# Performance work log

Measured on AMD Instinct MI355X. Metric: run time of the kernel, lower is better.

## Reference

```python
import jax, jax.numpy as jnp
import numpy as np

EPS_IN = 1e-5  # torch InstanceNorm1d default eps


def instance_norm(x):
    # x: [B, C, L]; normalize over L per (B, C); no affine (torch default)
    m = jnp.mean(x, axis=-1, keepdims=True)
    v = jnp.var(x, axis=-1, keepdims=True)
    return (x - m) / jnp.sqrt(v + EPS_IN)


def conv1x1(x, w, b):
    # x: [B, Cin, L], w: [Cout, Cin], b: [Cout]
    return jnp.einsum('bcl,oc->bol', x, w) + b[None, :, None]


def _window_indices(L_dec, L_enc, window, stride):
    # static (numpy) window layout matching the torch while-loop
    starts = list(range(0, L_dec, stride))
    dec_ends = [min(s + window, L_dec) for s in starts]
    enc_se = [(int(s * L_enc / L_dec), min(int(e * L_enc / L_dec), L_enc))
              for s, e in zip(starts, dec_ends)]
    max_enc = max(ee - es for es, ee in enc_se)
    ar_d = np.arange(window)
    ar_e = np.arange(max_enc)
    dec_idx = np.stack([np.clip(s + ar_d, 0, L_dec - 1) for s in starts])          # [NW, Wd]
    dec_valid = np.stack([(s + ar_d) < e for s, e in zip(starts, dec_ends)])       # [NW, Wd]
    enc_idx = np.stack([np.clip(es + ar_e, 0, L_enc - 1) for es, ee in enc_se])    # [NW, We]
    enc_valid = np.stack([(es + ar_e) < ee for es, ee in enc_se])                  # [NW, We]
    return (jnp.asarray(dec_idx), jnp.asarray(dec_valid),
            jnp.asarray(enc_idx), jnp.asarray(enc_valid))


def setup_inputs() -> dict:
    key = jax.random.key(0)
    ks = jax.random.split(key, 16)
    B, Cd, Ce, Ld, Le = 4, 512, 256, 4096, 8192
    H = 4 * Cd  # mlp hidden
    s = 0.02
    return {
        'x_decoder': jax.random.normal(ks[0], (B, Cd, Ld), jnp.float32),
        'x_encoder': jax.random.normal(ks[1], (B, Ce, Le), jnp.float32),
        'wq': jax.random.normal(ks[2], (Cd, Cd), jnp.float32) * s,
        'bq': jnp.zeros((Cd,), jnp.float32),
        'wk': jax.random.normal(ks[3], (Cd, Ce), jnp.float32) * s,
        'bk': jnp.zeros((Cd,), jnp.float32),
        'wv': jax.random.normal(ks[4], (Cd, Ce), jnp.float32) * s,
        'bv': jnp.zeros((Cd,), jnp.float32),
        'wo': jax.random.normal(ks[5], (Cd, Cd), jnp.float32) * s,
        'bo': jnp.zeros((Cd,), jnp.float32),
        'w1': jax.random.normal(ks[6], (H, Cd), jnp.float32) * s,
        'b1': jnp.zeros((H,), jnp.float32),
        'w2': jax.random.normal(ks[7], (Cd, H), jnp.float32) * s,
        'b2': jnp.zeros((Cd,), jnp.float32),
    }


NUM_HEADS = 8
WINDOW = 256
STRIDE = 192  # int(256 * (1 - 0.25))


def reference(x_decoder, x_encoder, wq, bq, wk, bk, wv, bv, wo, bo, w1, b1, w2, b2):
    B, Cd, Ld = x_decoder.shape
    Le = x_encoder.shape[-1]
    nh, hd = NUM_HEADS, Cd // NUM_HEADS
    residual = x_decoder

    q = instance_norm(conv1x1(x_decoder, wq, bq))
    k = instance_norm(conv1x1(x_encoder, wk, bk))
    v = instance_norm(conv1x1(x_encoder, wv, bv))

    # [B, C, L] -> [B, nh, L, hd]
    q = q.reshape(B, nh, hd, Ld).transpose(0, 1, 3, 2)
    k = k.reshape(B, nh, hd, Le).transpose(0, 1, 3, 2)
    v = v.reshape(B, nh, hd, Le).transpose(0, 1, 3, 2)

    dec_idx, dec_valid, enc_idx, enc_valid = _window_indices(Ld, Le, WINDOW, STRIDE)
    # gather all windows at once
    qw = q[:, :, dec_idx, :]  # [B, nh, NW, Wd, hd]
    kw = k[:, :, enc_idx, :]  # [B, nh, NW, We, hd]
    vw = v[:, :, enc_idx, :]

    scale = hd ** -0.5
    scores = jnp.einsum('bhnqd,bhnkd->bhnqk', qw, kw) * scale
    scores = jnp.where(enc_valid[None, None, :, None, :], scores, jnp.float32(-1e30))
    attn = jax.nn.softmax(scores, axis=-1)
    win = jnp.einsum('bhnqk,bhnkd->bhnqd', attn, vw)
    win = win * dec_valid[None, None, :, :, None].astype(win.dtype)

    # scatter-add overlapping windows then average by overlap count
    flat_idx = dec_idx.reshape(-1)  # [NW*Wd]
    out = jnp.zeros((B, nh, Ld, hd), win.dtype).at[:, :, flat_idx, :].add(
        win.reshape(B, nh, -1, hd))
    counts = jnp.zeros((Ld,), win.dtype).at[flat_idx].add(
        dec_valid.reshape(-1).astype(win.dtype))
    out = out / jnp.clip(counts, 1e-8)[None, None, :, None]

    attn_out = out.transpose(0, 1, 3, 2).reshape(B, Cd, Ld)
    x = instance_norm(conv1x1(attn_out, wo, bo)) + residual

    # AttentionMLP1D (dropout inactive in eval)
    h = jax.nn.gelu(conv1x1(x, w1, b1), approximate=False)
    y = instance_norm(conv1x1(h, w2, b2))
    return y + x
```

## Files before the change

### kernel.cpp

```cpp
#include <hip/hip_runtime.h>
#include <hip/hip_bf16.h>
#include <math.h>
#include <stdint.h>

#define LDD 4096
#define LEE 8192
#define CDIM 512
#define CENC 256
#define HDIM 2048
#define NB 4
#define NHEAD 8
#define HD 64
#define NWIN 22
#define WINQ 256
#define WSTRIDE 192

typedef __attribute__((ext_vector_type(8))) short bf16x8;
typedef __attribute__((ext_vector_type(8))) unsigned short u16x8;
typedef __attribute__((ext_vector_type(4))) float f32x4;
typedef __attribute__((ext_vector_type(16))) float f32x16;
typedef __attribute__((ext_vector_type(2))) unsigned int u32x2;
typedef __attribute__((ext_vector_type(4))) unsigned int u32x4;
typedef unsigned short ushort_t;

__device__ __forceinline__ uint32_t pack2(float lo, float hi) {
    return ((__float_as_uint(hi) + 0x8000u) & 0xffff0000u) |
           ((__float_as_uint(lo) + 0x8000u) >> 16);
}
__device__ __forceinline__ ushort_t bfc(float x) {
    return (ushort_t)((__float_as_uint(x) + 0x8000u) >> 16);
}
__device__ __forceinline__ float bf2f(ushort_t u) {
    return __uint_as_float(((uint32_t)u) << 16);
}
__device__ __forceinline__ void gload16(const void* g, void* l) {
    __builtin_amdgcn_global_load_lds(
        (const __attribute__((address_space(1))) void*)g,
        (__attribute__((address_space(3))) void*)l, 16, 0, 0);
}
__device__ __forceinline__ float gelu_fast(float x) {
    float z = fabsf(x) * 0.70710678f;
    float t = 1.0f / fmaf(0.3275911f, z, 1.0f);
    float p = t * fmaf(t, fmaf(t, fmaf(t, fmaf(t, 1.061405429f, -1.453152027f),
                                        1.421413741f), -0.284496736f), 0.254829592f);
    float e = __expf(-z * z);
    float erfz = fmaf(-p, e, 1.0f);
    float sgn = copysignf(erfz, x);
    return 0.5f * x * (1.0f + sgn);
}

struct Cvt6Args {
    const float* src[6];
    ushort_t* dst[6];
    int n[6];
};
__global__ __launch_bounds__(256)
void cvt6(Cvt6Args a)
{
    int seg = blockIdx.y;
    int i = (blockIdx.x * 256 + threadIdx.x) * 4;
    if (i < a.n[seg]) {
        float4 v = *reinterpret_cast<const float4*>(&a.src[seg][i]);
        u32x2 p; p[0] = pack2(v.x, v.y); p[1] = pack2(v.z, v.w);
        *reinterpret_cast<u32x2*>(&a.dst[seg][i]) = p;
    }
}

__global__ __launch_bounds__(256)
void tcvt(const float* __restrict__ in, ushort_t* __restrict__ outb, int C, int L)
{
    __shared__ float T[64][65];
    int l0 = blockIdx.x * 64, c0 = blockIdx.y * 64, b = blockIdx.z;
    int tid = threadIdx.x;
    int ll = tid & 63, cq = tid >> 6;
    #pragma unroll
    for (int i = 0; i < 16; ++i) {
        int c = cq + i * 4;
        T[c][ll] = in[((size_t)b * C + c0 + c) * L + l0 + ll];
    }
    __syncthreads();
    int cc = tid & 63, lq = tid >> 6;
    #pragma unroll
    for (int i = 0; i < 16; ++i) {
        int l = lq + i * 4;
        outb[((size_t)b * L + l0 + l) * C + c0 + cc] = bfc(T[cc][l]);
    }
}

template<int EPI, int STATS>
__global__ __launch_bounds__(256)
void mgemm2(const ushort_t* __restrict__ A, const ushort_t* __restrict__ Wt,
            const float* __restrict__ bias, ushort_t* __restrict__ Out,
            float* __restrict__ part, int M, int N, int K)
{
    __shared__ __align__(16) ushort_t As[2][8192];
    __shared__ __align__(16) ushort_t Bs[2][8192];

    int Nt = gridDim.x;
    int flat = blockIdx.y * Nt + blockIdx.x;
    int nwg = Nt * gridDim.y;
    int swz = (flat & 7) * (nwg >> 3) + (flat >> 3);
    int nb = swz % Nt, mb = swz / Nt;
    int b = blockIdx.z;
    int m0 = mb * 128, n0 = nb * 128;

    int tid = threadIdx.x;
    int lane = tid & 63;
    int w = tid >> 6;
    int q16 = lane & 15, g = lane >> 4;
    int wr = w >> 1, wc = w & 1;

    const ushort_t* Ag[4]; const ushort_t* Wg[4];
    #pragma unroll
    for (int i = 0; i < 4; ++i) {
        int gran = w * 256 + i * 64 + lane;
        int row = gran >> 3;
        int c8 = (gran & 7) ^ (row & 7);
        Ag[i] = A + ((size_t)b * M + m0 + row) * K + c8 * 8;
        Wg[i] = Wt + ((size_t)(n0 + row)) * K + c8 * 8;
    }

    f32x4 acc[4][4];
    #pragma unroll
    for (int mt = 0; mt < 4; ++mt)
        #pragma unroll
        for (int nt = 0; nt < 4; ++nt) {
            acc[mt][nt][0] = 0.f; acc[mt][nt][1] = 0.f;
            acc[mt][nt][2] = 0.f; acc[mt][nt][3] = 0.f;
        }

    #pragma unroll
    for (int i = 0; i < 4; ++i) {
        gload16(Ag[i], &As[0][w * 2048 + i * 512]);
        gload16(Wg[i], &Bs[0][w * 2048 + i * 512]);
    }

    int NTILES = K >> 6;
    for (int kt = 0; kt < NTILES; ++kt) {
        int cur = kt & 1;
        __syncthreads();
        if (kt + 1 < NTILES) {
            int k0 = (kt + 1) << 6;
            #pragma unroll
            for (int i = 0; i < 4; ++i) {
                gload16(Ag[i] + k0, &As[cur ^ 1][w * 2048 + i * 512]);
                gload16(Wg[i] + k0, &Bs[cur ^ 1][w * 2048 + i * 512]);
            }
        }
        const char* Ab = (const char*)&As[cur][0];
        const char* Bb = (const char*)&Bs[cur][0];
        bf16x8 ka[4][2], kb[4][2];
        #pragma unroll
        for (int mt = 0; mt < 4; ++mt) {
            int r = wr * 64 + mt * 16 + q16;
            int rb = r * 128;
            int sw8 = (r & 7) << 4;
            ka[mt][0] = *reinterpret_cast<const bf16x8*>(Ab + rb + ((g * 16) ^ sw8));
            ka[mt][1] = *reinterpret_cast<const bf16x8*>(Ab + rb + ((64 + g * 16) ^ sw8));
        }
        #pragma unroll
        for (int nt = 0; nt < 4; ++nt) {
            int r = wc * 64 + nt * 16 + q16;
            int rb = r * 128;
            int sw8 = (r & 7) << 4;
            kb[nt][0] = *reinterpret_cast<const bf16x8*>(Bb + rb + ((g * 16) ^ sw8));
            kb[nt][1] = *reinterpret_cast<const bf16x8*>(Bb + rb + ((64 + g * 16) ^ sw8));
        }
        #pragma unroll
        for (int mt = 0; mt < 4; ++mt)
            #pragma unroll
            for (int nt = 0; nt < 4; ++nt) {
                acc[mt][nt] = __builtin_amdgcn_mfma_f32_16x16x32_bf16(kb[nt][0], ka[mt][0], acc[mt][nt], 0, 0, 0);
                acc[mt][nt] = __builtin_amdgcn_mfma_f32_16x16x32_bf16(kb[nt][1], ka[mt][1], acc[mt][nt], 0, 0, 0);
            }
    }

    float4 bv4[4];
    #pragma unroll
    for (int nt = 0; nt < 4; ++nt)
        bv4[nt] = *reinterpret_cast<const float4*>(&bias[n0 + wc * 64 + nt * 16 + g * 4]);

    float s_[4][4], q_[4][4];
    if (STATS) {
        #pragma unroll
        for (int nt = 0; nt < 4; ++nt)
            #pragma unroll
            for (int r = 0; r < 4; ++r) { s_[nt][r] = 0.f; q_[nt][r] = 0.f; }
    }

    #pragma unroll
    for (int mt = 0; mt < 4; ++mt) {
        int m = m0 + wr * 64 + mt * 16 + q16;
        size_t rowoff = ((size_t)b * M + m) * N;
        #pragma unroll
        for (int nt = 0; nt < 4; ++nt) {
            float vv[4];
            #pragma unroll
            for (int r = 0; r < 4; ++r) {
                float val = acc[mt][nt][r] + ((const float*)&bv4[nt])[r];
                if (EPI == 1) val = gelu_fast(val);
                if (STATS) { s_[nt][r] += val; q_[nt][r] = fmaf(val, val, q_[nt][r]); }
                vv[r] = val;
            }
            u32x2 pk; pk[0] = pack2(vv[0], vv[1]); pk[1] = pack2(vv[2], vv[3]);
            *reinterpret_cast<u32x2*>(&Out[rowoff + n0 + wc * 64 + nt * 16 + g * 4]) = pk;
        }
    }

    if (STATS) {
        __syncthreads();
        float* SS = (float*)&As[0][0];
        float* SQ = (float*)&Bs[0][0];
        #pragma unroll
        for (int nt = 0; nt < 4; ++nt)
            #pragma unroll
            for (int r = 0; r < 4; ++r) {
                int nl = wc * 64 + nt * 16 + g * 4 + r;
                SS[nl * 33 + wr * 16 + q16] = s_[nt][r];
                SQ[nl * 33 + wr * 16 + q16] = q_[nt][r];
            }
        __syncthreads();
        if (tid < 128) {
            float ts = 0.f, tq = 0.f;
            #pragma unroll 8
            for (int j = 0; j < 32; ++j) { ts += SS[tid * 33 + j]; tq += SQ[tid * 33 + j]; }
            size_t po = (((size_t)b * (M >> 7) + mb) * N + n0 + tid) * 2;
            part[po] = ts; part[po + 1] = tq;
        }
    }
}

__global__ __launch_bounds__(256)
void stats_finish(const float* __restrict__ pk, const float* __restrict__ pv,
                  float* __restrict__ km, float* __restrict__ kr,
                  float* __restrict__ vm, float* __restrict__ vr)
{
    int id = blockIdx.x * 256 + threadIdx.x;
    int b = id >> 9, c = id & 511;
    float sk = 0.f, qk = 0.f, sv = 0.f, qv = 0.f;
    for (int sp = 0; sp < 64; ++sp) {
        size_t po = (((size_t)(b * 64 + sp)) * CDIM + c) * 2;
        sk += pk[po]; qk += pk[po + 1];
        sv += pv[po]; qv += pv[po + 1];
    }
    float mk = sk / (float)LEE, mv = sv / (float)LEE;
    km[id] = mk;
    kr[id] = rsqrtf(qk / (float)LEE - mk * mk + 1e-5f);
    vm[id] = mv;
    vr[id] = rsqrtf(qv / (float)LEE - mv * mv + 1e-5f);
}

template<int RES>
__global__ __launch_bounds__(256)
void cn_apply_v(const ushort_t* __restrict__ in, const float* __restrict__ part,
                const ushort_t* __restrict__ res, ushort_t* __restrict__ out,
                const float* __restrict__ chscale,
                int L, int SPLITM, float oscale)
{
    __shared__ float SM[CDIM], SR[CDIM];
    int b = blockIdx.z;
    int tid = threadIdx.x;
    for (int c = tid; c < CDIM; c += 256) {
        float fs = 0.f, fq = 0.f;
        for (int sp = 0; sp < SPLITM; ++sp) {
            size_t po = (((size_t)b * SPLITM + sp) * CDIM + c) * 2;
            fs += part[po]; fq += part[po + 1];
        }
        float mean = fs / (float)L;
        float var = fq / (float)L - mean * mean;
        float sc = oscale;
        if (chscale) sc *= chscale[b * CDIM + c];
        SM[c] = mean; SR[c] = rsqrtf(var + 1e-5f) * sc;
    }
    __syncthreads();
    int c0 = (tid & 63) * 8;
    int l0 = blockIdx.x * 16 + (tid >> 6) * 4;
    float mm[8], rr[8];
    #pragma unroll
    for (int j = 0; j < 8; ++j) { mm[j] = SM[c0 + j]; rr[j] = SR[c0 + j]; }
    #pragma unroll
    for (int i = 0; i < 4; ++i) {
        int l = l0 + i;
        size_t off = ((size_t)b * L + l) * CDIM + c0;
        u16x8 v = *reinterpret_cast<const u16x8*>(in + off);
        u16x8 rv;
        if (RES) rv = *reinterpret_cast<const u16x8*>(res + off);
        u16x8 o;
        #pragma unroll
        for (int j = 0; j < 8; ++j) {
            float y = (bf2f((ushort_t)v[j]) - mm[j]) * rr[j];
            if (RES) y += bf2f((ushort_t)rv[j]);
            o[j] = bfc(y);
        }
        *reinterpret_cast<u16x8*>(out + off) = o;
    }
}

__global__ __launch_bounds__(256)
void cn_apply_t(const ushort_t* __restrict__ in, const float* __restrict__ part,
                const ushort_t* __restrict__ res, float* __restrict__ outf,
                int L, int SPLITM)
{
    __shared__ float SM[64], SR[64];
    __shared__ float T[64][65];
    int b = blockIdx.z;
    int c0 = blockIdx.x * 64;
    int l0 = blockIdx.y * 64;
    int tid = threadIdx.x;
    if (tid < 64) {
        int c = c0 + tid;
        float fs = 0.f, fq = 0.f;
        for (int sp = 0; sp < SPLITM; ++sp) {
            size_t po = (((size_t)b * SPLITM + sp) * CDIM + c) * 2;
            fs += part[po]; fq += part[po + 1];
        }
        float mean = fs / (float)L;
        float var = fq / (float)L - mean * mean;
        SM[tid] = mean; SR[tid] = rsqrtf(var + 1e-5f);
    }
    __syncthreads();
    int cc = tid & 63;
    int lq = tid >> 6;
    float mean = SM[cc], rstd = SR[cc];
    #pragma unroll
    for (int i = 0; i < 16; ++i) {
        int l = l0 + lq + i * 4;
        size_t idx = ((size_t)b * L + l) * CDIM + c0 + cc;
        T[lq + i * 4][cc] = (bf2f(in[idx]) - mean) * rstd + bf2f(res[idx]);
    }
    __syncthreads();
    int ll = tid & 63;
    int cr = tid >> 6;
    #pragma unroll
    for (int i = 0; i < 16; ++i) {
        int c = cr + i * 4;
        outf[((size_t)b * CDIM + c0 + c) * L + l0 + ll] = T[ll][c];
    }
}

__global__ __launch_bounds__(512, 2)
void attn_win_mfma32(const ushort_t* __restrict__ qT, const ushort_t* __restrict__ kT,
                     const ushort_t* __restrict__ vT,
                     const float* __restrict__ vmean, const float* __restrict__ vrstd,
                     ushort_t* __restrict__ win)
{
    __shared__ __align__(16) char KB[2][16384];
    __shared__ __align__(16) ushort_t VBv[2][64][132];
    __shared__ float VMS[64], VRS[64];

    int p = blockIdx.x;
    int xcd = p & 7;
    int sub = p >> 3;
    int g9 = xcd * 11 + (sub % 11);
    int hh = sub / 11;
    int n = g9 % 22, b = g9 / 22;

    int s = n * WSTRIDE;
    int es = 2 * s;
    bool tail = (n == NWIN - 1);
    int nch = tail ? 1 : 4;

    int tid = threadIdx.x;
    int lane = tid & 63;
    int w = tid >> 6;
    int l31 = lane & 31;
    int hf = lane >> 5;
    bool active = (!tail) || (w < 2);

    if (tid < 64) {
        int c = b * CDIM + hh * HD + tid;
        VMS[tid] = vmean[c];
        VRS[tid] = vrstd[c];
    }

    const ushort_t* kbase = kT + ((size_t)b * LEE + es) * CDIM + hh * HD;
    const ushort_t* vbase = vT + ((size_t)b * LEE + es) * CDIM + hh * HD;

    int vc8 = tid & 7;
    int vkp2 = tid >> 3;

    {
        #pragma unroll
        for (int i = 0; i < 2; ++i) {
            int gr = tid + i * 512;
            int kpos = gr >> 3;
            int c8 = (gr & 7) ^ (kpos & 7);
            gload16(kbase + (size_t)kpos * CDIM + c8 * 8, &KB[0][gr * 16]);
        }
        const ushort_t* src = vbase + (size_t)(2 * vkp2) * CDIM + vc8 * 8;
        u16x8 wa = *reinterpret_cast<const u16x8*>(src);
        u16x8 wb = *reinterpret_cast<const u16x8*>(src + CDIM);
        #pragma unroll
        for (int j = 0; j < 8; ++j) {
            int d = vc8 * 8 + j;
            uint32_t dw = (uint32_t)wa[j] | ((uint32_t)wb[j] << 16);
            *reinterpret_cast<uint32_t*>(&VBv[0][d][2 * vkp2]) = dw;
        }
    }

    bf16x8 bq[4];
    if (active) {
        int qrow_g = s + w * 32 + l31;
        const ushort_t* qp = qT + ((size_t)b * LDD + qrow_g) * CDIM + hh * HD;
        #pragma unroll
        for (int kd = 0; kd < 4; ++kd)
            bq[kd] = *reinterpret_cast<const bf16x8*>(qp + kd * 16 + hf * 8);
    }

    f32x16 acc0, acc1;
    #pragma unroll
    for (int e = 0; e < 16; ++e) { acc0[e] = 0.f; acc1[e] = 0.f; }
    float m = -3e38f, ssum = 0.f;
    int swk = (lane & 7) << 4;

    for (int ch = 0; ch < nch; ++ch) {
        int buf = ch & 1;
        __syncthreads();

        u16x8 wa, wb;
        bool pf = (ch + 1 < nch);
        if (pf) {
            #pragma unroll
            for (int i = 0; i < 2; ++i) {
                int gr = tid + i * 512;
                int kpos = gr >> 3;
                int c8 = (gr & 7) ^ (kpos & 7);
                gload16(kbase + (size_t)((ch + 1) * 128 + kpos) * CDIM + c8 * 8,
                        &KB[buf ^ 1][gr * 16]);
            }
            const ushort_t* src = vbase + (size_t)((ch + 1) * 128 + 2 * vkp2) * CDIM + vc8 * 8;
            wa = *reinterpret_cast<const u16x8*>(src);
            wb = *reinterpret_cast<const u16x8*>(src + CDIM);
        }

        if (active) {
            #pragma unroll 1
            for (int ccl = 0; ccl < 2; ++ccl) {
                f32x16 st0, st1;
                #pragma unroll
                for (int e = 0; e < 16; ++e) { st0[e] = 0.f; st1[e] = 0.f; }
                const char* KA0 = &KB[buf][(ccl * 64 + l31) * 128];
                const char* KA1 = KA0 + 32 * 128;
                __builtin_amdgcn_s_setprio(1);
                #pragma unroll
                for (int kd = 0; kd < 4; ++kd) {
                    int co = (kd * 32 + hf * 16) ^ swk;
                    bf16x8 ka0 = *reinterpret_cast<const bf16x8*>(KA0 + co);
                    bf16x8 ka1 = *reinterpret_cast<const bf16x8*>(KA1 + co);
                    st0 = __builtin_amdgcn_mfma_f32_32x32x16_bf16(ka0, bq[kd], st0, 0, 0, 0);
                    st1 = __builtin_amdgcn_mfma_f32_32x32x16_bf16(ka1, bq[kd], st1, 0, 0, 0);
                }
                __builtin_amdgcn_s_setprio(0);
                float pmax = st0[0];
                #pragma unroll
                for (int e = 1; e < 16; ++e) pmax = fmaxf(pmax, st0[e]);
                #pragma unroll
                for (int e = 0; e < 16; ++e) pmax = fmaxf(pmax, st1[e]);
                pmax = fmaxf(pmax, __shfl_xor(pmax, 32));
                if (!__all(pmax <= m + 11.5f)) {
                    float mnew = fmaxf(m, pmax);
                    float corr = exp2f(m - mnew);
                    m = mnew;
                    ssum *= corr;
                    #pragma unroll
                    for (int e = 0; e < 16; ++e) { acc0[e] *= corr; acc1[e] *= corr; }
                }
                uint32_t pk0[8], pk1[8];
                float ls = 0.f;
                #pragma unroll
                for (int pp = 0; pp < 8; ++pp) {
                    float a = exp2f(st0[2 * pp] - m), bb = exp2f(st0[2 * pp + 1] - m);
                    float c = exp2f(st1[2 * pp] - m), dd = exp2f(st1[2 * pp + 1] - m);
                    ls += (a + bb) + (c + dd);
                    pk0[pp] = pack2(a, bb);
                    pk1[pp] = pack2(c, dd);
                }
                ssum += ls;
                __builtin_amdgcn_s_setprio(1);
                #pragma unroll
                for (int kc = 0; kc < 4; ++kc) {
                    const int sub2 = kc & 1;
                    uint32_t pA0, pA1, pA2, pA3;
                    if ((kc >> 1) == 0) { pA0 = pk0[4*sub2]; pA1 = pk0[4*sub2+1]; pA2 = pk0[4*sub2+2]; pA3 = pk0[4*sub2+3]; }
                    else                { pA0 = pk1[4*sub2]; pA1 = pk1[4*sub2+1]; pA2 = pk1[4*sub2+2]; pA3 = pk1[4*sub2+3]; }
                    uint32_t s0 = hf ? pA0 : pA2;
                    uint32_t s1 = hf ? pA1 : pA3;
                    uint32_t r0 = (uint32_t)__shfl_xor((int)s0, 32);
                    uint32_t r1 = (uint32_t)__shfl_xor((int)s1, 32);
                    u32x4 bt;
                    bt[0] = hf ? r0 : pA0;
                    bt[1] = hf ? r1 : pA1;
                    bt[2] = hf ? pA2 : r0;
                    bt[3] = hf ? pA3 : r1;
                    bf16x8 pbf = __builtin_bit_cast(bf16x8, bt);
                    int ko = ccl * 64 + kc * 16 + hf * 8;
                    const uint32_t* vr0 = reinterpret_cast<const uint32_t*>(&VBv[buf][l31][ko]);
                    const uint32_t* vr1 = reinterpret_cast<const uint32_t*>(&VBv[buf][l31 + 32][ko]);
                    u32x2 alo = *reinterpret_cast<const u32x2*>(vr0);
                    u32x2 ahi = *reinterpret_cast<const u32x2*>(vr0 + 2);
                    u32x2 blo = *reinterpret_cast<const u32x2*>(vr1);
                    u32x2 bhi = *reinterpret_cast<const u32x2*>(vr1 + 2);
                    u32x4 va0u, va1u;
                    va0u[0] = alo[0]; va0u[1] = alo[1]; va0u[2] = ahi[0]; va0u[3] = ahi[1];
                    va1u[0] = blo[0]; va1u[1] = blo[1]; va1u[2] = bhi[0]; va1u[3] = bhi[1];
                    bf16x8 va0 = __builtin_bit_cast(bf16x8, va0u);
                    bf16x8 va1 = __builtin_bit_cast(bf16x8, va1u);
                    acc0 = __builtin_amdgcn_mfma_f32_32x32x16_bf16(va0, pbf, acc0, 0, 0, 0);
                    acc1 = __builtin_amdgcn_mfma_f32_32x32x16_bf16(va1, pbf, acc1, 0, 0, 0);
                }
                __builtin_amdgcn_s_setprio(0);
            }
        }

        if (pf) {
            #pragma unroll
            for (int j = 0; j < 8; ++j) {
                int d = vc8 * 8 + j;
                uint32_t dw = (uint32_t)wa[j] | ((uint32_t)wb[j] << 16);
                *reinterpret_cast<uint32_t*>(&VBv[buf ^ 1][d][2 * vkp2]) = dw;
            }
        }
    }

    if (active) {
        float stot = ssum + __shfl_xor(ssum, 32);
        float rs = 1.f / stot;
        size_t wbase = (((size_t)(b * NHEAD + hh) * NWIN + n) * WINQ + (size_t)(w * 32 + l31)) * HD;
        #pragma unroll
        for (int p4 = 0; p4 < 4; ++p4) {
            int d0 = p4 * 8 + hf * 4;
            float o0[4], o1[4];
            #pragma unroll
            for (int e = 0; e < 4; ++e) {
                o0[e] = VRS[d0 + e] * (acc0[4 * p4 + e] * rs - VMS[d0 + e]);
                o1[e] = VRS[32 + d0 + e] * (acc1[4 * p4 + e] * rs - VMS[32 + d0 + e]);
            }
            u32x2 w0, w1v;
            w0[0] = pack2(o0[0], o0[1]); w0[1] = pack2(o0[2], o0[3]);
            w1v[0] = pack2(o1[0], o1[1]); w1v[1] = pack2(o1[2], o1[3]);
            *reinterpret_cast<u32x2*>(&win[wbase + p4 * 8 + hf * 4]) = w0;
            *reinterpret_cast<u32x2*>(&win[wbase + 32 + p4 * 8 + hf * 4]) = w1v;
        }
    }
}

__global__ __launch_bounds__(256)
void attn_finalize(const ushort_t* __restrict__ win, ushort_t* __restrict__ outT)
{
    int l0 = blockIdx.x * 64;
    int hh = blockIdx.y, b = blockIdx.z;
    int tid = threadIdx.x;
    int d2 = tid & 31;
    int lq = tid >> 5;
    #pragma unroll
    for (int i = 0; i < 8; ++i) {
        int ll = lq + i * 8;
        int l = l0 + ll;
        int n1 = min(NWIN - 1, l / WSTRIDE);
        int n0 = (l >= 64) ? ((l - 64) / WSTRIDE) : 0;
        float a0 = 0.f, a1 = 0.f;
        for (int nn = n0; nn <= n1; ++nn) {
            int qrow = l - nn * WSTRIDE;
            uint32_t v = *reinterpret_cast<const uint32_t*>(
                &win[(((size_t)(b * NHEAD + hh) * NWIN + nn) * WINQ + qrow) * HD + d2 * 2]);
            a0 += bf2f((ushort_t)(v & 0xffffu));
            a1 += bf2f((ushort_t)(v >> 16));
        }
        float inv = 1.f / (float)(n1 - n0 + 1);
        uint32_t o = pack2(a0 * inv, a1 * inv);
        *reinterpret_cast<uint32_t*>(
            &outT[((size_t)b * LDD + l) * CDIM + hh * HD + d2 * 2]) = o;
    }
}

extern "C" void kernel_launch(void* const* d_in, const int* in_sizes, int n_in,
                              void* d_out, int out_size, void* d_ws, size_t ws_size,
                              hipStream_t stream)
{
    const float* x_dec = (const float*)d_in[0];
    const float* x_enc = (const float*)d_in[1];
    const float* wq = (const float*)d_in[2];
    const float* bq = (const float*)d_in[3];
    const float* wk = (const float*)d_in[4];
    const float* bk = (const float*)d_in[5];
    const float* wv = (const float*)d_in[6];
    const float* bv = (const float*)d_in[7];
    const float* wo = (const float*)d_in[8];
    const float* bo = (const float*)d_in[9];
    const float* w1 = (const float*)d_in[10];
    const float* b1 = (const float*)d_in[11];
    const float* w2 = (const float*)d_in[12];
    const float* b2 = (const float*)d_in[13];
    float* out = (float*)d_out;

    char* base = (char*)d_ws;
    ushort_t* wqb = (ushort_t*)(base);
    ushort_t* wkb = (ushort_t*)(base + 524288);
    ushort_t* wvb = (ushort_t*)(base + 786432);
    ushort_t* wob = (ushort_t*)(base + 1048576);
    ushort_t* w1b = (ushort_t*)(base + 1572864);
    ushort_t* w2b = (ushort_t*)(base + 3670016);
    ushort_t* x_decT_b = (ushort_t*)(base + 5767168);
    ushort_t* q_pre    = (ushort_t*)(base + 22544384);
    ushort_t* k_pre    = (ushort_t*)(base + 39321600);
    ushort_t* v_pre    = (ushort_t*)(base + 72876032);
    ushort_t* x_encT_b = (ushort_t*)(base + 106430464);
    ushort_t* winb     = (ushort_t*)(base + 123207680);
    float*    partQ    = (float*)(base + 169345024);
    float*    partK    = (float*)(base + 170393600);
    float*    partV    = (float*)(base + 171442176);
    float*    km       = (float*)(base + 172490752);
    float*    krs      = km + 2048;
    float*    vm       = krs + 2048;
    float*    vrs      = vm + 2048;
    ushort_t* attn_outT = x_encT_b;
    ushort_t* xo_pre   = q_pre;
    ushort_t* hT       = k_pre;
    ushort_t* y_pre    = winb;

    dim3 blk(256);

    Cvt6Args ca;
    ca.src[0] = wq; ca.src[1] = wk; ca.src[2] = wv;
    ca.src[3] = wo; ca.src[4] = w1; ca.src[5] = w2;
    ca.dst[0] = wqb; ca.dst[1] = wkb; ca.dst[2] = wvb;
    ca.dst[3] = wob; ca.dst[4] = w1b; ca.dst[5] = w2b;
    ca.n[0] = 262144; ca.n[1] = 131072; ca.n[2] = 131072;
    ca.n[3] = 262144; ca.n[4] = 1048576; ca.n[5] = 1048576;
    cvt6<<<dim3(1024, 6), blk, 0, stream>>>(ca);

    tcvt<<<dim3(LDD / 64, CDIM / 64, NB), blk, 0, stream>>>(x_dec, x_decT_b, CDIM, LDD);
    tcvt<<<dim3(LEE / 64, CENC / 64, NB), blk, 0, stream>>>(x_enc, x_encT_b, CENC, LEE);

    const float QSCALE = 0.125f * 1.4426950408889634f;

    mgemm2<0,1><<<dim3(CDIM / 128, LDD / 128, NB), blk, 0, stream>>>(x_decT_b, wqb, bq, q_pre, partQ, LDD, CDIM, CDIM);
    mgemm2<0,1><<<dim3(CDIM / 128, LEE / 128, NB), blk, 0, stream>>>(x_encT_b, wkb, bk, k_pre, partK, LEE, CDIM, CENC);
    mgemm2<0,1><<<dim3(CDIM / 128, LEE / 128, NB), blk, 0, stream>>>(x_encT_b, wvb, bv, v_pre, partV, LEE, CDIM, CENC);
    stats_finish<<<dim3(8), blk, 0, stream>>>(partK, partV, km, krs, vm, vrs);

    cn_apply_v<0><<<dim3(LDD / 16, 1, NB), blk, 0, stream>>>(q_pre, partQ, nullptr, q_pre, krs, LDD, LDD / 128, QSCALE);

    attn_win_mfma32<<<dim3(NWIN * NHEAD * NB), dim3(512), 0, stream>>>(q_pre, k_pre, v_pre, vm, vrs, winb);
    attn_finalize<<<dim3(LDD / 64, NHEAD, NB), blk, 0, stream>>>(winb, attn_outT);

    mgemm2<0,1><<<dim3(CDIM / 128, LDD / 128, NB), blk, 0, stream>>>(attn_outT, wob, bo, xo_pre, partQ, LDD, CDIM, CDIM);
    cn_apply_v<1><<<dim3(LDD / 16, 1, NB), blk, 0, stream>>>(xo_pre, partQ, x_decT_b, xo_pre, nullptr, LDD, LDD / 128, 1.0f);

    mgemm2<1,0><<<dim3(HDIM / 128, LDD / 128, NB), blk, 0, stream>>>(xo_pre, w1b, b1, hT, nullptr, LDD, HDIM, CDIM);

    mgemm2<0,1><<<dim3(CDIM / 128, LDD / 128, NB), blk, 0, stream>>>(hT, w2b, b2, y_pre, partQ, LDD, CDIM, HDIM);
    cn_apply_t<<<dim3(CDIM / 64, LDD / 64, NB), blk, 0, stream>>>(y_pre, partQ, xo_pre, out, LDD, LDD / 128);

    (void)in_sizes; (void)n_in; (void)out_size; (void)ws_size;
}
```

Before: 354.1 us.

## Enlarge GEMM tile to 256 rows with 512 threads and triple-buffered LDS pipeline

Replaces the 128x128 double-buffered GEMM with a 256x128 tile run by 8 waves per block. It adds a three-stage LDS ring with explicit vmcnt waits and a single barrier per k-step, so global loads run two tiles ahead of the MFMA work. The statistics partials and their consumers are updated for the halved M split count. This aims to hide load latency and reuse weight tiles across more rows, at the cost of larger LDS use (about 144KB), one block per CU, and fewer blocks for the smaller GEMMs.

```diff
diff --git a/kernel.cpp b/kernel.cpp
--- a/kernel.cpp
+++ b/kernel.cpp
@@ -88,13 +88,13 @@
 }
 
 template<int EPI, int STATS>
-__global__ __launch_bounds__(256)
-void mgemm2(const ushort_t* __restrict__ A, const ushort_t* __restrict__ Wt,
+__global__ __launch_bounds__(512, 1)
+void mgemm3(const ushort_t* __restrict__ A, const ushort_t* __restrict__ Wt,
             const float* __restrict__ bias, ushort_t* __restrict__ Out,
             float* __restrict__ part, int M, int N, int K)
 {
-    __shared__ __align__(16) ushort_t As[2][8192];
-    __shared__ __align__(16) ushort_t Bs[2][8192];
+    __shared__ __align__(16) ushort_t As[3][16384];
+    __shared__ __align__(16) ushort_t Bs[3][8192];
 
     int Nt = gridDim.x;
     int flat = blockIdx.y * Nt + blockIdx.x;
@@ -102,7 +102,7 @@
     int swz = (flat & 7) * (nwg >> 3) + (flat >> 3);
     int nb = swz % Nt, mb = swz / Nt;
     int b = blockIdx.z;
-    int m0 = mb * 128, n0 = nb * 128;
+    int m0 = mb * 256, n0 = nb * 128;
 
     int tid = threadIdx.x;
     int lane = tid & 63;
@@ -110,15 +110,31 @@
     int q16 = lane & 15, g = lane >> 4;
     int wr = w >> 1, wc = w & 1;
 
-    const ushort_t* Ag[4]; const ushort_t* Wg[4];
+    const ushort_t* Ag[4];
     #pragma unroll
     for (int i = 0; i < 4; ++i) {
         int gran = w * 256 + i * 64 + lane;
         int row = gran >> 3;
         int c8 = (gran & 7) ^ (row & 7);
         Ag[i] = A + ((size_t)b * M + m0 + row) * K + c8 * 8;
+    }
+    const ushort_t* Wg[2];
+    #pragma unroll
+    for (int i = 0; i < 2; ++i) {
+        int gran = w * 128 + i * 64 + lane;
+        int row = gran >> 3;
+        int c8 = (gran & 7) ^ (row & 7);
         Wg[i] = Wt + ((size_t)(n0 + row)) * K + c8 * 8;
     }
+
+    auto STAGE = [&](int buf, int k0) {
+        #pragma unroll
+        for (int i = 0; i < 4; ++i)
+            gload16(Ag[i] + k0, &As[buf][w * 2048 + i * 512]);
+        #pragma unroll
+        for (int i = 0; i < 2; ++i)
+            gload16(Wg[i] + k0, &Bs[buf][w * 1024 + i * 512]);
+    };
 
     f32x4 acc[4][4];
     #pragma unroll
@@ -129,26 +145,20 @@
             acc[mt][nt][2] = 0.f; acc[mt][nt][3] = 0.f;
         }
 
-    #pragma unroll
-    for (int i = 0; i < 4; ++i) {
-        gload16(Ag[i], &As[0][w * 2048 + i * 512]);
-        gload16(Wg[i], &Bs[0][w * 2048 + i * 512]);
-    }
-
-    int NTILES = K >> 6;
-    for (int kt = 0; kt < NTILES; ++kt) {
-        int cur = kt & 1;
-        __syncthreads();
-        if (kt + 1 < NTILES) {
-            int k0 = (kt + 1) << 6;
-            #pragma unroll
-            for (int i = 0; i < 4; ++i) {
-                gload16(Ag[i] + k0, &As[cur ^ 1][w * 2048 + i * 512]);
-                gload16(Wg[i] + k0, &Bs[cur ^ 1][w * 2048 + i * 512]);
-            }
-        }
-        const char* Ab = (const char*)&As[cur][0];
-        const char* Bb = (const char*)&Bs[cur][0];
+    int NT = K >> 6;
+    STAGE(0, 0);
+    STAGE(1, 64);
+
+    for (int kt = 0; kt < NT; ++kt) {
+        int buf = kt % 3;
+        if (kt < NT - 1) asm volatile("s_waitcnt vmcnt(6)" ::: "memory");
+        else             asm volatile("s_waitcnt vmcnt(0)" ::: "memory");
+        __builtin_amdgcn_s_barrier();
+        asm volatile("" ::: "memory");
+        if (kt + 2 < NT) STAGE((kt + 2) % 3, (kt + 2) * 64);
+
+        const char* Ab = (const char*)&As[buf][0];
+        const char* Bb = (const char*)&Bs[buf][0];
         bf16x8 ka[4][2], kb[4][2];
         #pragma unroll
         for (int mt = 0; mt < 4; ++mt) {
@@ -210,21 +220,21 @@
     if (STATS) {
         __syncthreads();
         float* SS = (float*)&As[0][0];
-        float* SQ = (float*)&Bs[0][0];
+        float* SQ = SS + 128 * 65;
         #pragma unroll
         for (int nt = 0; nt < 4; ++nt)
             #pragma unroll
             for (int r = 0; r < 4; ++r) {
                 int nl = wc * 64 + nt * 16 + g * 4 + r;
-                SS[nl * 33 + wr * 16 + q16] = s_[nt][r];
-                SQ[nl * 33 + wr * 16 + q16] = q_[nt][r];
+                SS[nl * 65 + wr * 16 + q16] = s_[nt][r];
+                SQ[nl * 65 + wr * 16 + q16] = q_[nt][r];
             }
         __syncthreads();
         if (tid < 128) {
             float ts = 0.f, tq = 0.f;
             #pragma unroll 8
-            for (int j = 0; j < 32; ++j) { ts += SS[tid * 33 + j]; tq += SQ[tid * 33 + j]; }
-            size_t po = (((size_t)b * (M >> 7) + mb) * N + n0 + tid) * 2;
+            for (int j = 0; j < 64; ++j) { ts += SS[tid * 65 + j]; tq += SQ[tid * 65 + j]; }
+            size_t po = (((size_t)b * (M >> 8) + mb) * N + n0 + tid) * 2;
             part[po] = ts; part[po + 1] = tq;
         }
     }
@@ -233,13 +243,13 @@
 __global__ __launch_bounds__(256)
 void stats_finish(const float* __restrict__ pk, const float* __restrict__ pv,
                   float* __restrict__ km, float* __restrict__ kr,
-                  float* __restrict__ vm, float* __restrict__ vr)
+                  float* __restrict__ vm, float* __restrict__ vr, int SPLIT)
 {
     int id = blockIdx.x * 256 + threadIdx.x;
     int b = id >> 9, c = id & 511;
     float sk = 0.f, qk = 0.f, sv = 0.f, qv = 0.f;
-    for (int sp = 0; sp < 64; ++sp) {
-        size_t po = (((size_t)(b * 64 + sp)) * CDIM + c) * 2;
+    for (int sp = 0; sp < SPLIT; ++sp) {
+        size_t po = (((size_t)(b * SPLIT + sp)) * CDIM + c) * 2;
         sk += pk[po]; qk += pk[po + 1];
         sv += pv[po]; qv += pv[po + 1];
     }
@@ -619,6 +629,7 @@
     ushort_t* y_pre    = winb;
 
     dim3 blk(256);
+    dim3 blk512(512);
 
     Cvt6Args ca;
     ca.src[0] = wq; ca.src[1] = wk; ca.src[2] = wv;
@@ -634,23 +645,23 @@
 
     const float QSCALE = 0.125f * 1.4426950408889634f;
 
-    mgemm2<0,1><<<dim3(CDIM / 128, LDD / 128, NB), blk, 0, stream>>>(x_decT_b, wqb, bq, q_pre, partQ, LDD, CDIM, CDIM);
-    mgemm2<0,1><<<dim3(CDIM / 128, LEE / 128, NB), blk, 0, stream>>>(x_encT_b, wkb, bk, k_pre, partK, LEE, CDIM, CENC);
-    mgemm2<0,1><<<dim3(CDIM / 128, LEE / 128, NB), blk, 0, stream>>>(x_encT_b, wvb, bv, v_pre, partV, LEE, CDIM, CENC);
-    stats_finish<<<dim3(8), blk, 0, stream>>>(partK, partV, km, krs, vm, vrs);
-
-    cn_apply_v<0><<<dim3(LDD / 16, 1, NB), blk, 0, stream>>>(q_pre, partQ, nullptr, q_pre, krs, LDD, LDD / 128, QSCALE);
-
-    attn_win_mfma32<<<dim3(NWIN * NHEAD * NB), dim3(512), 0, stream>>>(q_pre, k_pre, v_pre, vm, vrs, winb);
+    mgemm3<0,1><<<dim3(CDIM / 128, LDD / 256, NB), blk512, 0, stream>>>(x_decT_b, wqb, bq, q_pre, partQ, LDD, CDIM, CDIM);
+    mgemm3<0,1><<<dim3(CDIM / 128, LEE / 256, NB), blk512, 0, stream>>>(x_encT_b, wkb, bk, k_pre, partK, LEE, CDIM, CENC);
+    mgemm3<0,1><<<dim3(CDIM / 128, LEE / 256, NB), blk512, 0, stream>>>(x_encT_b, wvb, bv, v_pre, partV, LEE, CDIM, CENC);
+    stats_finish<<<dim3(8), blk, 0, stream>>>(partK, partV, km, krs, vm, vrs, LEE / 256);
+
+    cn_apply_v<0><<<dim3(LDD / 16, 1, NB), blk, 0, stream>>>(q_pre, partQ, nullptr, q_pre, krs, LDD, LDD / 256, QSCALE);
+
+    attn_win_mfma32<<<dim3(NWIN * NHEAD * NB), blk512, 0, stream>>>(q_pre, k_pre, v_pre, vm, vrs, winb);
     attn_finalize<<<dim3(LDD / 64, NHEAD, NB), blk, 0, stream>>>(winb, attn_outT);
 
-    mgemm2<0,1><<<dim3(CDIM / 128, LDD / 128, NB), blk, 0, stream>>>(attn_outT, wob, bo, xo_pre, partQ, LDD, CDIM, CDIM);
-    cn_apply_v<1><<<dim3(LDD / 16, 1, NB), blk, 0, stream>>>(xo_pre, partQ, x_decT_b, xo_pre, nullptr, LDD, LDD / 128, 1.0f);
-
-    mgemm2<1,0><<<dim3(HDIM / 128, LDD / 128, NB), blk, 0, stream>>>(xo_pre, w1b, b1, hT, nullptr, LDD, HDIM, CDIM);
-
-    mgemm2<0,1><<<dim3(CDIM / 128, LDD / 128, NB), blk, 0, stream>>>(hT, w2b, b2, y_pre, partQ, LDD, CDIM, HDIM);
-    cn_apply_t<<<dim3(CDIM / 64, LDD / 64, NB), blk, 0, stream>>>(y_pre, partQ, xo_pre, out, LDD, LDD / 128);
+    mgemm3<0,1><<<dim3(CDIM / 128, LDD / 256, NB), blk512, 0, stream>>>(attn_outT, wob, bo, xo_pre, partQ, LDD, CDIM, CDIM);
+    cn_apply_v<1><<<dim3(LDD / 16, 1, NB), blk, 0, stream>>>(xo_pre, partQ, x_decT_b, xo_pre, nullptr, LDD, LDD / 256, 1.0f);
+
+    mgemm3<1,0><<<dim3(HDIM / 128, LDD / 256, NB), blk512, 0, stream>>>(xo_pre, w1b, b1, hT, nullptr, LDD, HDIM, CDIM);
+
+    mgemm3<0,1><<<dim3(CDIM / 128, LDD / 256, NB), blk512, 0, stream>>>(hT, w2b, b2, y_pre, partQ, LDD, CDIM, HDIM);
+    cn_apply_t<<<dim3(CDIM / 64, LDD / 64, NB), blk, 0, stream>>>(y_pre, partQ, xo_pre, out, LDD, LDD / 256);
 
     (void)in_sizes; (void)n_in; (void)out_size; (void)ws_size;
 }
```

After: 366.1 us. 3.4% more time.
